# Kernel tuning notes

Measured on AMD Instinct MI355X. Metric: run time of the kernel, lower is better.

Reference implementation:

```python
import math
import jax
import jax.numpy as jnp
import numpy as np
from jax import lax

D_MODEL = 256
N = 64
L = 2048
BATCH = 8
DT = 0.1


def setup_inputs() -> dict:
    key = jax.random.key(0)
    k1, k2, k3, k4 = jax.random.split(key, 4)
    n2 = N // 2
    # Faithful parameter init from _init_parameters
    A_real = jnp.log(jnp.ones((D_MODEL, n2), jnp.float32) * 0.5)
    A_imag = jnp.broadcast_to(jnp.arange(n2, dtype=jnp.float32) * math.pi, (D_MODEL, n2))
    C_real = jax.random.normal(k1, (D_MODEL, n2), jnp.float32)
    C_imag = jax.random.normal(k2, (D_MODEL, n2), jnp.float32)
    D = jnp.zeros((D_MODEL,), jnp.float32)
    u = jax.random.normal(k3, (BATCH, L, D_MODEL), jnp.float32)
    return {"u": u, "A_real": A_real, "A_imag": A_imag,
            "C_real": C_real, "C_imag": C_imag, "D": D}


def reference(u, A_real, A_imag, C_real, C_imag, D):
    batch, Lseq, d_model = u.shape
    # A = -exp(A_real) + i*A_imag ; discretize: A_disc = exp(A * dt)
    A = (-jnp.exp(A_real) + 1j * A_imag).astype(jnp.complex64)
    A_disc = jnp.exp(A * DT)  # (d, n/2) complex
    C = (C_real + 1j * C_imag).astype(jnp.complex64)  # (d, n/2)
    # torch.fft.rfftfreq(2L, 1/L) = arange(L+1) / 2
    freqs = jnp.arange(Lseq + 1, dtype=jnp.float32) * 0.5
    omega = jnp.exp((-2j * math.pi) * freqs.astype(jnp.complex64) / Lseq)  # (L+1,)
    # Cauchy-like sum over modes: (d, n/2, L+1) -> (d, L+1)
    k_f = (C[:, :, None] / (1.0 - omega[None, None, :] * A_disc[:, :, None])).sum(axis=1)
    # irfft to length 2L, keep first L taps -> depthwise conv kernel (d, L)
    k = jnp.fft.irfft(k_f, n=2 * Lseq, axis=-1)[:, :Lseq].astype(u.dtype)
    pad_left = (Lseq - 1) // 2
    pad_right =Seq = Lseq // 2
    uT = jnp.transpose(u, (0, 2, 1))  # (B, d, L)
    # torch conv1d == cross-correlation == lax conv (no kernel flip)
    y = lax.conv_general_dilated(
        uT, k[:, None, :],  # (d, 1, L) depthwise kernel
        window_strides=(1,), padding=[(pad_left, pad_right)],
        feature_group_count=d_model,
        dimension_numbers=("NCH", "OIH", "NCH"))
    y = y + D[None, :, None]
    return jnp.transpose(y, (0, 2, 1))  # (B, L, d)
```

## Files before the change

### kernel.cpp

```cpp
#include <hip/hip_runtime.h>
#include <hip/hip_bf16.h>
#include <math.h>

#define LSEQ   2048
#define DMODEL 256
#define NHALF  32
#define TMAX   1024
#define TM2    384
#define KPAD   16
#define KROWS  (LSEQ + 2*KPAD)
#define TT     16

typedef __attribute__((ext_vector_type(8))) short short8;
typedef __attribute__((ext_vector_type(4))) short short4v;
typedef __attribute__((ext_vector_type(4))) float f32x4;
typedef __attribute__((ext_vector_type(4))) unsigned int u32x4;

#define U3STR   2136
#define U3SH    (8*U3STR)
#define U3BYTES (U3SH*2)
#define KSLOT_STR 8848
#define OFF_K    U3BYTES
#define SMEM_F3  (OFF_K + 8*KSLOT_STR)
#define KBF_SH   4400
#define YTR_SMEM (64*260*4)
#define YSWZ(r)  ((((r) >> 2) & 7) << 2)
#define UIMG_SHORTS ((size_t)DMODEL*U3SH)
#define KBF_OFF_SH  UIMG_SHORTS
#define YT_OFF_B    ((UIMG_SHORTS + (size_t)DMODEL*KBF_SH)*2)
#define WS_NEED3    (YT_OFF_B + (size_t)8*LSEQ*DMODEL*2)

#define PB_CT0 0
#define PB_CT1 4928
#define PB_HRE 9856
#define PB_HIE 11392
#define PB_HIO 12160
#define PB_P   12928
#define PB_Q   17280
#define PB_C   23808
#define PB_BYTES 33792

__global__ __launch_bounds__(512, 2) void s4d_prep(
    const float* __restrict__ u,
    const float* __restrict__ A_real, const float* __restrict__ A_imag,
    const float* __restrict__ C_real, const float* __restrict__ C_imag,
    unsigned short* __restrict__ uimg, unsigned short* __restrict__ kbf)
{
    __shared__ __align__(16) unsigned char pbuf[PB_BYTES];
    const int tid = threadIdx.x;

    if (blockIdx.y < 8) {
        unsigned short (*tr)[66] = (unsigned short (*)[66])pbuf;
        const int m0 = blockIdx.x * 64;
        const int b  = blockIdx.y;

        const int mmBase = tid >> 6;
        const int d4     = (tid & 63) * 4;
        #pragma unroll
        for (int it = 0; it < 8; ++it) {
            int mm = it*8 + mmBase;
            const float* src = u + ((size_t)b*LSEQ + m0 + mm)*DMODEL + d4;
            f32x4 v = *(const f32x4*)src;
            #pragma unroll
            for (int j = 0; j < 4; ++j) {
                __hip_bfloat16 hb = __float2bfloat16(v[j]);
                tr[d4+j][mm] = *(unsigned short*)&hb;
            }
        }
        __syncthreads();
        #pragma unroll
        for (int P = 0; P < 4; ++P) {
            int d = P*64 + (tid >> 3);
            int c = tid & 7;
            const unsigned short* s = &tr[d][c*8];
            u32x4 w = { *(const unsigned*)(s),   *(const unsigned*)(s+2),
                        *(const unsigned*)(s+4), *(const unsigned*)(s+6) };
            *(u32x4*)(uimg + (size_t)d*U3SH + (size_t)b*U3STR + 32 + m0 + c*8) = w;
        }
        if (blockIdx.x == 0 && tid < 256) {
            int d = tid;
            #pragma unroll
            for (int c = 0; c < 4; ++c)
                *(u32x4*)(uimg + (size_t)d*U3SH + (size_t)b*U3STR + c*8) = (u32x4){0,0,0,0};
        } else if (blockIdx.x == 31 && tid < 256) {
            int d = tid;
            #pragma unroll
            for (int c = 0; c < 7; ++c)
                *(u32x4*)(uimg + (size_t)d*U3SH + (size_t)b*U3STR + 2080 + c*8) = (u32x4){0,0,0,0};
        }
    } else {
        const int d = (blockIdx.y - 8)*32 + blockIdx.x;
        float* ctL0 = (float*)(pbuf + PB_CT0);
        float* ctL1 = (float*)(pbuf + PB_CT1);
        float* hRe  = (float*)(pbuf + PB_HRE);
        float* hImE = (float*)(pbuf + PB_HIE);
        float* hImO = (float*)(pbuf + PB_HIO);
        float* Pp   = (float*)(pbuf + PB_P);
        float* Qp   = (float*)(pbuf + PB_Q);
        float* Cp   = (float*)(pbuf + PB_C);

        for (int i = tid; i < 1220; i += 512) {
            int x0 = (i - 196) & 2047;
            int x1 = (i - 195) & 2047;
            float a0 = (float)(M_PI/(2.0*(double)LSEQ)) * (float)(2*x0 + 1);
            float a1 = (float)(M_PI/(2.0*(double)LSEQ)) * (float)(2*x1 + 1);
            float s0, c0, s1, c1;
            sincosf(a0, &s0, &c0);
            sincosf(a1, &s1, &c1);
            ctL0[i] = c0 / s0;
            ctL1[i] = c1 / s1;
        }
        if (tid < 32) {
            const int n = tid;
            float ar = A_real[d*NHALF + n], ai = A_imag[d*NHALF + n];
            float cr = C_real[d*NHALF + n], ci = C_imag[d*NHALF + n];
            float amp = expf(-0.1f * expf(ar));
            float sn, cs; sincosf(0.1f * ai, &sn, &cs);
            float Adr = amp*cs, Adi = amp*sn;
            float pr = 1.f, pi = 0.f;
            Pp[n*2] = pr; Pp[n*2 + 1] = pi;
            #pragma unroll
            for (int i = 1; i < 16; ++i) {
                float nr = pr*Adr - pi*Adi;
                float ni = pr*Adi + pi*Adr;
                pr = nr; pi = ni;
                Pp[i*68 + n*2] = pr; Pp[i*68 + n*2 + 1] = pi;
            }
            float a16r = pr*Adr - pi*Adi;
            float a16i = pr*Adi + pi*Adr;
            float qr = 1.f, qi = 0.f;
            Qp[n*2] = qr; Qp[n*2 + 1] = qi;
            #pragma unroll
            for (int j = 1; j < 24; ++j) {
                float nr = qr*a16r - qi*a16i;
                float ni = qr*a16i + qi*a16r;
                qr = nr; qi = ni;
                Qp[j*68 + n*2] = qr; Qp[j*68 + n*2 + 1] = qi;
            }
            Cp[n*2] = cr; Cp[n*2 + 1] = ci;
        }
        __syncthreads();

        if (tid < TM2) {
            const int tau = tid, ii = tau & 15, jj = tau >> 4;
            const float* Pr = Pp + ii*68;
            const float* Qr = Qp + jj*68;
            float aR = 0.f, aI = 0.f;
            #pragma unroll 4
            for (int n = 0; n < 32; n += 2) {
                f32x4 p = *(const f32x4*)(Pr + 2*n);
                f32x4 q = *(const f32x4*)(Qr + 2*n);
                f32x4 c = *(const f32x4*)(Cp + 2*n);
                float w0r = p[0]*q[0] - p[1]*q[1];
                float w0i = p[0]*q[1] + p[1]*q[0];
                aR = fmaf(c[0], w0r, aR); aR = fmaf(-c[1], w0i, aR);
                aI = fmaf(c[0], w0i, aI); aI = fmaf( c[1], w0r, aI);
                float w1r = p[2]*q[2] - p[3]*q[3];
                float w1i = p[2]*q[3] + p[3]*q[2];
                aR = fmaf(c[2], w1r, aR); aR = fmaf(-c[3], w1i, aR);
                aI = fmaf(c[2], w1i, aI); aI = fmaf( c[3], w1r, aI);
            }
            hRe[tau] = aR;
            if (tau & 1) hImO[tau >> 1] = aI;
            else         hImE[tau >> 1] = aI;
        }
        __syncthreads();

        unsigned short* kd = kbf + (size_t)d*KBF_SH;
        {
            const int pt = tid & 1;
            const int g  = tid >> 1;
            float accs[4] = {0.f, 0.f, 0.f, 0.f};

            if (g < 128) {
                const float* tb = pt ? ctL1 : ctL0;
                const float* hb = pt ? hImE : hImO;
                float acc0 = 0.f, acc1 = 0.f, acc2 = 0.f, acc3 = 0.f;
                int qb = 4*g + 192;
                f32x4 Wlo = *(const f32x4*)(tb + qb);
                f32x4 Whi = *(const f32x4*)(tb + qb + 4);

                #pragma unroll 4
                for (int R = 0; R < 48; ++R) {
                    f32x4 hv = *(const f32x4*)(hb + 4*R);
                    f32x4 Wn = *(const f32x4*)(tb + qb - 4);
                    acc0 = fmaf(Wlo[3], hv[0], acc0); acc1 = fmaf(Whi[0], hv[0], acc1);
                    acc2 = fmaf(Whi[1], hv[0], acc2); acc3 = fmaf(Whi[2], hv[0], acc3);
                    acc0 = fmaf(Wlo[2], hv[1], acc0); acc1 = fmaf(Wlo[3], hv[1], acc1);
                    acc2 = fmaf(Whi[0], hv[1], acc2); acc3 = fmaf(Whi[1], hv[1], acc3);
                    acc0 = fmaf(Wlo[1], hv[2], acc0); acc1 = fmaf(Wlo[2], hv[2], acc1);
                    acc2 = fmaf(Wlo[3], hv[2], acc2); acc3 = fmaf(Whi[0], hv[2], acc3);
                    acc0 = fmaf(Wlo[0], hv[3], acc0); acc1 = fmaf(Wlo[1], hv[3], acc1);
                    acc2 = fmaf(Wlo[2], hv[3], acc2); acc3 = fmaf(Wlo[3], hv[3], acc3);
                    Whi = Wlo; Wlo = Wn; qb -= 4;
                }
                accs[0] = acc0; accs[1] = acc1; accs[2] = acc2; accs[3] = acc3;
            }
            #pragma unroll
            for (int e = 0; e < 4; ++e) {
                int t = 8*g + 2*e + pt;
                unsigned short us = 0;
                if (t < 1024) {
                    float base = (t < TM2) ? hRe[t] : 0.f;
                    float kv = base - accs[e] * (1.0f/(float)LSEQ);
                    __hip_bfloat16 hbv = __float2bfloat16(kv);
                    us = *(unsigned short*)&hbv;
                }
                kd[1056 + t] = us;
            }
        }
        if (tid < 132) *(u32x4*)((unsigned char*)kd + tid*16) = (u32x4){0,0,0,0};
        if (tid < 162) *(u32x4*)((unsigned char*)kd + 6208 + tid*16) = (u32x4){0,0,0,0};
    }
}

#define MF(a, b, c) __builtin_amdgcn_mfma_f32_16x16x32_bf16((a), (b), (c), 0, 0, 0)

#define BODY(P) do {                                                        \
    const short8 bcur = Bb[(P) & 3];                                        \
    Bb[((P)+2) & 3] = *(const short8*)(sm + aBn);                           \
    acc[7] = MF(A[((P)+1) & 7], bcur, acc[7]);                              \
    A[((P)+1) & 7] = *(const short8*)(sm + aAn);                            \
    aAn += 64; aBn += 64;                                                   \
    acc[6] = MF(A[((P)+2) & 7], bcur, acc[6]);                              \
    acc[5] = MF(A[((P)+3) & 7], bcur, acc[5]);                              \
    acc[4] = MF(A[((P)+4) & 7], bcur, acc[4]);                              \
    acc[3] = MF(A[((P)+5) & 7], bcur, acc[3]);                              \
    acc[2] = MF(A[((P)+6) & 7], bcur, acc[2]);                              \
    acc[1] = MF(A[((P)+7) & 7], bcur, acc[1]);                              \
    acc[0] = MF(A[(P) & 7],     bcur, acc[0]);                              \
} while (0)

__global__ __launch_bounds__(512, 1) void s4d_mfma9(
    const unsigned short* __restrict__ uimg, const unsigned short* __restrict__ kbf,
    const float* __restrict__ Dvec, unsigned short* __restrict__ yTb)
{
    extern __shared__ __align__(16) unsigned char sm[];
    const int tid = threadIdx.x;
    const int Bk  = blockIdx.x;
    const int d   = ((Bk & 7) << 5) | (Bk >> 3);

    const u32x4* gu = (const u32x4*)(uimg + (size_t)d*U3SH);
    const u32x4* gk = (const u32x4*)(kbf + (size_t)d*KBF_SH);
    u32x4 stg[5], kst[2];
    #pragma unroll
    for (int r = 0; r < 5; ++r) {
        int i = tid + 512*r;
        if (i < U3SH/8) stg[r] = gu[i];
    }
    #pragma unroll
    for (int r = 0; r < 2; ++r) {
        int i = tid + 512*r;
        if (i < KBF_SH/8) kst[r] = gk[i];
    }
    #pragma unroll
    for (int r = 0; r < 2; ++r) {
        int i = tid + 512*r;
        if (i < KBF_SH/8) *(u32x4*)(sm + OFF_K + i*16) = kst[r];
    }
    __syncthreads();

    {
        const unsigned short* s0p = (const unsigned short*)(sm + OFF_K);
        for (int i = tid; i < 548; i += 512) {
            int z0 = i*8;
            u32x4 va = *(const u32x4*)(s0p + z0);
            u32x4 vb = *(const u32x4*)(s0p + z0 + 8);
            unsigned src[8] = { va[0], va[1], va[2], va[3],
                                vb[0], vb[1], vb[2], vb[3] };
            #pragma unroll
            for (int c = 1; c < 8; ++c) {
                u32x4 w;
                if ((c & 1) == 0) {
                    int q = c >> 1;
                    w = (u32x4){ src[q], src[q+1], src[q+2], src[q+3] };
                } else {
                    int q = (c - 1) >> 1;
                    w = (u32x4){ (src[q]   >> 16) | (src[q+1] << 16),
                                 (src[q+1] >> 16) | (src[q+2] << 16),
                                 (src[q+2] >> 16) | (src[q+3] << 16),
                                 (src[q+3] >> 16) | (src[q+4] << 16) };
                }
                *(u32x4*)(sm + OFF_K + c*KSLOT_STR + z0*2) = w;
            }
        }
    }
    #pragma unroll
    for (int r = 0; r < 5; ++r) {
        int i = tid + 512*r;
        if (i < U3SH/8) *(u32x4*)(sm + i*16) = stg[r];
    }
    __syncthreads();

    const int lane = tid & 63, wv = tid >> 6;
    const int h    = lane >> 4;
    const int col  = lane & 15;
    const int t0w  = wv << 8;

    const int cA   = (7 - col) & 7;
    const int bA0  = OFF_K + cA*KSLOT_STR + 2*(2047 + 8*h - col - cA - t0w);
    const int laneB3 = (col & 7)*(U3STR*2) + 64 + 16*h + 32*(col >> 3);

    const int qs   = (wv > 4) ? 8*(wv - 4) : 0;
    const int nOut = (wv < 4) ? (wv + 1) : 5;

    const int bA0s = bA0 + 64*qs;
    const int lB3s = laneB3 + 64*qs;

    const float dv = Dvec[d];
    f32x4 acc[8];
    #pragma unroll
    for (int j = 0; j < 8; ++j) acc[j] = (f32x4){dv, dv, dv, dv};

    short8 A[8], Bb[4];
    #pragma unroll
    for (int w = 0; w < 8; ++w)
        A[w] = *(const short8*)(sm + bA0s - 64*((8 - w) & 7));
    Bb[0] = *(const short8*)(sm + lB3s - 64);
    Bb[1] = *(const short8*)(sm + lB3s);

    int aAn = bA0s + 64;
    int aBn = lB3s + 64;

    BODY(0);
    for (int o = 0; o < nOut; ++o) {
        BODY(1); BODY(2); BODY(3); BODY(4);
        BODY(5); BODY(6); BODY(7); BODY(0);
    }

    {
        const int b    = col & 7;
        const int hi16 = (col >> 3) << 4;
        unsigned short* yb = yTb + (size_t)d*(8*LSEQ) + (size_t)b*LSEQ;
        #pragma unroll
        for (int j = 0; j < 8; ++j) {
            int trow = t0w + 32*j + hi16 + 4*h;
            short4v pk;
            #pragma unroll
            for (int e = 0; e < 4; ++e) {
                __hip_bfloat16 hb = __float2bfloat16(acc[j][e]);
                pk[e] = *(short*)&hb;
            }
            *(short4v*)(yb + trow) = pk;
        }
    }
}

__global__ __launch_bounds__(256) void s4d_ytr(const unsigned short* __restrict__ yTb,
                                               float* __restrict__ out)
{
    extern __shared__ float tr2[];
    const int tid = threadIdx.x;
    const int t0  = blockIdx.x * 64;
    const int b   = blockIdx.y;

    const int g = tid >> 4, i = tid & 15;
    #pragma unroll
    for (int dp = 0; dp < 16; ++dp) {
        int dd = dp*16 + g;
        short4v v = *(const short4v*)(yTb + (size_t)dd*(8*LSEQ) + (size_t)b*LSEQ + t0 + i*4);
        #pragma unroll
        for (int e = 0; e < 4; ++e) {
            int r = i*4 + e;
            unsigned uv = ((unsigned)(unsigned short)v[e]) << 16;
            tr2[(r*260 + dd) ^ YSWZ(r)] = *(float*)&uv;
        }
    }
    __syncthreads();
    const int d4 = (tid & 63)*4, ttB = tid >> 6;
    #pragma unroll
    for (int s = 0; s < 16; ++s) {
        int tt = s*4 + ttB;
        f32x4 w = *(const f32x4*)(tr2 + ((tt*260 + d4) ^ YSWZ(tt)));
        *(f32x4*)(out + ((size_t)b*LSEQ + t0 + tt)*DMODEL + d4) = w;
    }
}

__global__ __launch_bounds__(256) void s4d_build_k(
    const float* __restrict__ A_real, const float* __restrict__ A_imag,
    const float* __restrict__ C_real, const float* __restrict__ C_imag,
    float* __restrict__ kT)
{
    __shared__ float hRe[TMAX], hIm[TMAX], ct[LSEQ], prm[4][NHALF];
    const int tid = threadIdx.x;
    const int d   = blockIdx.x;
    if (tid < NHALF) {
        prm[0][tid] = A_real[d*NHALF + tid];
        prm[1][tid] = A_imag[d*NHALF + tid];
        prm[2][tid] = C_real[d*NHALF + tid];
        prm[3][tid] = C_imag[d*NHALF + tid];
    }
    #pragma unroll
    for (int r = 0; r < LSEQ/256; ++r) {
        int i = tid + 256*r;
        float ang = (float)(M_PI/(2.0*(double)LSEQ)) * (float)(2*i + 1);
        float sv, cv; sincosf(ang, &sv, &cv);
        ct[i] = cv / sv;
    }
    __syncthreads();
    for (int r = 0; r < TMAX/256; ++r) {
        int tau = tid + 256*r;
        float aR = 0.f, aI = 0.f;
        for (int n = 0; n < NHALF; ++n) {
            float lr  = -expf(prm[0][n]) * 0.1f;
            float amp = expf(lr * (float)tau);
            double ph = (double)prm[1][n] * 0.1 * (double)tau;
            ph -= floor(ph * (1.0/(2.0*M_PI))) * (2.0*M_PI);
            float sv, cv; sincosf((float)ph, &sv, &cv);
            float cr = prm[2][n], ci = prm[3][n];
            aR = fmaf(amp, cr*cv - ci*sv, aR);
            aI = fmaf(amp, cr*sv + ci*cv, aI);
        }
        hRe[tau] = aR; hIm[tau] = aI;
    }
    __syncthreads();
    float base[8], hsum[8];
    #pragma unroll
    for (int r = 0; r < 8; ++r) {
        base[r] = (r < 4) ? hRe[tid + 256*r] : 0.f;
        hsum[r] = 0.f;
    }
    const int tau0 = (tid & 1) ^ 1;
    for (int tau = tau0; tau < TMAX; tau += 2) {
        float him = hIm[tau];
        #pragma unroll
        for (int r = 0; r < 8; ++r) {
            int idx = ((tid + 256*r - tau) & (2*LSEQ - 1)) >> 1;
            hsum[r] = fmaf(ct[idx], him, hsum[r]);
        }
    }
    #pragma unroll
    for (int r = 0; r < 8; ++r) {
        int t = tid + 256*r;
        kT[(t + KPAD)*DMODEL + d] = base[r] - hsum[r] * (1.0f/(float)LSEQ);
    }
    if (tid < 2*KPAD) {
        int row = (tid < KPAD) ? tid : (LSEQ + KPAD + (tid - KPAD));
        kT[row*DMODEL + d] = 0.f;
    }
}

__global__ __launch_bounds__(256) void s4d_conv(
    const float* __restrict__ u, const float* __restrict__ Dvec,
    const float* __restrict__ kT, float* __restrict__ out)
{
    const int d  = threadIdx.x;
    const int t0 = blockIdx.x * TT;
    const int b  = blockIdx.y;
    float dvv = Dvec[d];
    float acc[TT];
    #pragma unroll
    for (int i = 0; i < TT; ++i) acc[i] = dvv;
    const float* ub   = u + (size_t)b * LSEQ * DMODEL + d;
    const float* kcol = kT + d;
    int mstart = t0 - 1024; if (mstart < 0) mstart = 0;
    int mend   = t0 + 1040; if (mend > LSEQ) mend = LSEQ;
    float kreg[31];
    {
        int jpb = mstart - t0 + 1024;
        #pragma unroll
        for (int r = 0; r < 31; ++r) kreg[r] = kcol[(jpb + r)*DMODEL];
    }
    for (int m0 = mstart; m0 < mend; m0 += TT) {
        float ureg[TT];
        #pragma unroll
        for (int mm = 0; mm < TT; ++mm) ureg[mm] = ub[(m0 + mm)*DMODEL];
        float knew[TT];
        if (m0 + TT < mend) {
            int jnb = m0 - t0 + 1024 + 31;
            #pragma unroll
            for (int r = 0; r < TT; ++r) knew[r] = kcol[(jnb + r)*DMODEL];
        } else {
            #pragma unroll
            for (int r = 0; r < TT; ++r) knew[r] = 0.f;
        }
        #pragma unroll
        for (int mm = 0; mm < TT; ++mm)
            #pragma unroll
            for (int tt = 0; tt < TT; ++tt)
                acc[tt] = fmaf(ureg[mm], kreg[mm - tt + 15], acc[tt]);
        #pragma unroll
        for (int r = 0; r < 15; ++r) kreg[r] = kreg[r + 16];
        #pragma unroll
        for (int r = 0; r < 16; ++r) kreg[15 + r] = knew[r];
    }
    float* ob = out + ((size_t)b * LSEQ + t0) * DMODEL + d;
    #pragma unroll
    for (int tt = 0; tt < TT; ++tt) ob[tt*DMODEL] = acc[tt];
}

extern "C" void kernel_launch(void* const* d_in, const int* in_sizes, int n_in,
                              void* d_out, int out_size, void* d_ws, size_t ws_size,
                              hipStream_t stream)
{
    const float* u  = (const float*)d_in[0];
    const float* Ar = (const float*)d_in[1];
    const float* Ai = (const float*)d_in[2];
    const float* Cr = (const float*)d_in[3];
    const float* Ci = (const float*)d_in[4];
    const float* Dv = (const float*)d_in[5];
    float* out = (float*)d_out;
    int B = in_sizes[0] / (LSEQ * DMODEL);

    if (B == 8 && ws_size >= WS_NEED3) {
        unsigned short* uimg = (unsigned short*)d_ws;
        unsigned short* kbf  = uimg + KBF_OFF_SH;
        unsigned short* yTb  = (unsigned short*)((unsigned char*)d_ws + YT_OFF_B);
        hipFuncSetAttribute((const void*)s4d_mfma9,
                            hipFuncAttributeMaxDynamicSharedMemorySize, SMEM_F3);
        hipFuncSetAttribute((const void*)s4d_ytr,
                            hipFuncAttributeMaxDynamicSharedMemorySize, YTR_SMEM);
        s4d_prep<<<dim3(32, 16), 512, 0, stream>>>(u, Ar, Ai, Cr, Ci, uimg, kbf);
        s4d_mfma9<<<DMODEL, 512, SMEM_F3, stream>>>(uimg, kbf, Dv, yTb);
        s4d_ytr<<<dim3(LSEQ/64, 8), 256, YTR_SMEM, stream>>>(yTb, out);
    } else {
        float* kT = (float*)d_ws;
        s4d_build_k<<<DMODEL, 256, 0, stream>>>(Ar, Ai, Cr, Ci, kT);
        s4d_conv<<<dim3(LSEQ/TT, B), 256, 0, stream>>>(u, Dv, kT, out);
    }
}
```

Before: 32.25 us.

## Split per-channel MFMA conv across two 256-thread blocks with trimmed kernel staging

The conv kernel is relaunched as 512 blocks of 256 threads, two per channel, and each block handles half of the output time tiles instead of one 512-thread block per channel. Each block stages only the slice of the shifted kernel copies it needs, starting at an offset, which shrinks the shared-memory footprint. The launch bound now asks for two blocks per CU. The aim is better load balance and occupancy across CUs. The cost is that the full u image is loaded twice per channel, once by each block, which adds global-memory and LDS traffic.

```diff
diff --git a/kernel.cpp b/kernel.cpp
--- a/kernel.cpp
+++ b/kernel.cpp
@@ -19,12 +19,15 @@
 #define U3STR   2136
 #define U3SH    (8*U3STR)
 #define U3BYTES (U3SH*2)
-#define KSLOT_STR 8848
-#define OFF_K    U3BYTES
-#define SMEM_F3  (OFF_K + 8*KSLOT_STR)
-#define KBF_SH   4400
+#define KBF_SH  4400
 #define YTR_SMEM (64*260*4)
 #define YSWZ(r)  ((((r) >> 2) & 7) << 2)
+#define ZB       768
+#define KSLOT2   3472
+#define OFF_K2   U3BYTES
+#define SMEM_F5  (OFF_K2 + 8*KSLOT2 + 128)
+#define NSTAGE_G 218
+#define NEXP_G   216
 #define UIMG_SHORTS ((size_t)DMODEL*U3SH)
 #define KBF_OFF_SH  UIMG_SHORTS
 #define YT_OFF_B    ((UIMG_SHORTS + (size_t)DMODEL*KBF_SH)*2)
@@ -231,78 +234,70 @@
     acc[0] = MF(A[(P) & 7],     bcur, acc[0]);                              \
 } while (0)
 
-__global__ __launch_bounds__(512, 1) void s4d_mfma9(
+__global__ __launch_bounds__(256, 2) void s4d_mfma11(
     const unsigned short* __restrict__ uimg, const unsigned short* __restrict__ kbf,
     const float* __restrict__ Dvec, unsigned short* __restrict__ yTb)
 {
     extern __shared__ __align__(16) unsigned char sm[];
-    const int tid = threadIdx.x;
-    const int Bk  = blockIdx.x;
-    const int d   = ((Bk & 7) << 5) | (Bk >> 3);
+    const int tid  = threadIdx.x;
+    const int v    = ((blockIdx.x & 7) << 6) | (blockIdx.x >> 3);
+    const int d    = v >> 1;
+    const int half = v & 1;
 
     const u32x4* gu = (const u32x4*)(uimg + (size_t)d*U3SH);
-    const u32x4* gk = (const u32x4*)(kbf + (size_t)d*KBF_SH);
-    u32x4 stg[5], kst[2];
-    #pragma unroll
-    for (int r = 0; r < 5; ++r) {
-        int i = tid + 512*r;
+    const u32x4* gk = (const u32x4*)(kbf + (size_t)d*KBF_SH + ZB);
+    u32x4 stg[9];
+    #pragma unroll
+    for (int r = 0; r < 9; ++r) {
+        int i = tid + 256*r;
         if (i < U3SH/8) stg[r] = gu[i];
     }
-    #pragma unroll
-    for (int r = 0; r < 2; ++r) {
-        int i = tid + 512*r;
-        if (i < KBF_SH/8) kst[r] = gk[i];
-    }
-    #pragma unroll
-    for (int r = 0; r < 2; ++r) {
-        int i = tid + 512*r;
-        if (i < KBF_SH/8) *(u32x4*)(sm + OFF_K + i*16) = kst[r];
-    }
+    u32x4 kst = (tid < NSTAGE_G) ? gk[tid] : (u32x4){0,0,0,0};
+    if (tid < NSTAGE_G) *(u32x4*)(sm + OFF_K2 + tid*16) = kst;
     __syncthreads();
 
-    {
-        const unsigned short* s0p = (const unsigned short*)(sm + OFF_K);
-        for (int i = tid; i < 548; i += 512) {
-            int z0 = i*8;
-            u32x4 va = *(const u32x4*)(s0p + z0);
-            u32x4 vb = *(const u32x4*)(s0p + z0 + 8);
-            unsigned src[8] = { va[0], va[1], va[2], va[3],
-                                vb[0], vb[1], vb[2], vb[3] };
-            #pragma unroll
-            for (int c = 1; c < 8; ++c) {
-                u32x4 w;
-                if ((c & 1) == 0) {
-                    int q = c >> 1;
-                    w = (u32x4){ src[q], src[q+1], src[q+2], src[q+3] };
-                } else {
-                    int q = (c - 1) >> 1;
-                    w = (u32x4){ (src[q]   >> 16) | (src[q+1] << 16),
-                                 (src[q+1] >> 16) | (src[q+2] << 16),
-                                 (src[q+2] >> 16) | (src[q+3] << 16),
-                                 (src[q+3] >> 16) | (src[q+4] << 16) };
-                }
-                *(u32x4*)(sm + OFF_K + c*KSLOT_STR + z0*2) = w;
-            }
-        }
-    }
-    #pragma unroll
-    for (int r = 0; r < 5; ++r) {
-        int i = tid + 512*r;
+    if (tid < NEXP_G) {
+        const unsigned short* s0p = (const unsigned short*)(sm + OFF_K2);
+        int z0 = tid*8;
+        u32x4 va = *(const u32x4*)(s0p + z0);
+        u32x4 vb = *(const u32x4*)(s0p + z0 + 8);
+        unsigned src[8] = { va[0], va[1], va[2], va[3],
+                            vb[0], vb[1], vb[2], vb[3] };
+        #pragma unroll
+        for (int c = 1; c < 8; ++c) {
+            u32x4 w;
+            if ((c & 1) == 0) {
+                int q = c >> 1;
+                w = (u32x4){ src[q], src[q+1], src[q+2], src[q+3] };
+            } else {
+                int q = (c - 1) >> 1;
+                w = (u32x4){ (src[q]   >> 16) | (src[q+1] << 16),
+                             (src[q+1] >> 16) | (src[q+2] << 16),
+                             (src[q+2] >> 16) | (src[q+3] << 16),
+                             (src[q+3] >> 16) | (src[q+4] << 16) };
+            }
+            *(u32x4*)(sm + OFF_K2 + c*KSLOT2 + z0*2) = w;
+        }
+    }
+    #pragma unroll
+    for (int r = 0; r < 9; ++r) {
+        int i = tid + 256*r;
         if (i < U3SH/8) *(u32x4*)(sm + i*16) = stg[r];
     }
     __syncthreads();
 
     const int lane = tid & 63, wv = tid >> 6;
+    const int w8   = half*4 + wv;
     const int h    = lane >> 4;
     const int col  = lane & 15;
-    const int t0w  = wv << 8;
+    const int t0w  = w8 << 8;
 
     const int cA   = (7 - col) & 7;
-    const int bA0  = OFF_K + cA*KSLOT_STR + 2*(2047 + 8*h - col - cA - t0w);
+    const int bA0  = OFF_K2 + cA*KSLOT2 + 2*(2047 + 8*h - col - cA - t0w - ZB);
     const int laneB3 = (col & 7)*(U3STR*2) + 64 + 16*h + 32*(col >> 3);
 
-    const int qs   = (wv > 4) ? 8*(wv - 4) : 0;
-    const int nOut = (wv < 4) ? (wv + 1) : 5;
+    const int qs   = (w8 > 4) ? 8*(w8 - 4) : 0;
+    const int nOut = (w8 < 4) ? (w8 + 1) : 5;
 
     const int bA0s = bA0 + 64*qs;
     const int lB3s = laneB3 + 64*qs;
@@ -506,12 +501,12 @@
         unsigned short* uimg = (unsigned short*)d_ws;
         unsigned short* kbf  = uimg + KBF_OFF_SH;
         unsigned short* yTb  = (unsigned short*)((unsigned char*)d_ws + YT_OFF_B);
-        hipFuncSetAttribute((const void*)s4d_mfma9,
-                            hipFuncAttributeMaxDynamicSharedMemorySize, SMEM_F3);
+        hipFuncSetAttribute((const void*)s4d_mfma11,
+                            hipFuncAttributeMaxDynamicSharedMemorySize, SMEM_F5);
         hipFuncSetAttribute((const void*)s4d_ytr,
                             hipFuncAttributeMaxDynamicSharedMemorySize, YTR_SMEM);
         s4d_prep<<<dim3(32, 16), 512, 0, stream>>>(u, Ar, Ai, Cr, Ci, uimg, kbf);
-        s4d_mfma9<<<DMODEL, 512, SMEM_F3, stream>>>(uimg, kbf, Dv, yTb);
+        s4d_mfma11<<<512, 256, SMEM_F5, stream>>>(uimg, kbf, Dv, yTb);
         s4d_ytr<<<dim3(LSEQ/64, 8), 256, YTR_SMEM, stream>>>(yTb, out);
     } else {
         float* kT = (float*)d_ws;
```

After: 32.34 us. No clear change (+0.3%).
